# Optimization experiments

Measured on AMD Instinct MI355X. Metric: run time of the kernel, lower is better.

## Reference

```python
import jax, jax.numpy as jnp
import numpy as np

N_MICS = 192
OVERLAP = 1024
WINDOW = 524288
SPEED_OF_SOUND = 343000.0  # mm/s
FS = 768000.0


def setup_inputs() -> dict:
    key = jax.random.key(0)
    k1, k2, k3 = jax.random.split(key, 3)
    pos = jax.random.normal(k1, (1, 3), dtype=jnp.float32) * 100.0 + jnp.array([[363.0, -344.0, 1607.0]], dtype=jnp.float32)
    mic_pos = jax.random.uniform(k2, (N_MICS, 3), dtype=jnp.float32) * 100.0  # mm, spread ~100mm -> delays << OVERLAP
    buffer = jax.random.normal(k3, (N_MICS, OVERLAP + WINDOW), dtype=jnp.float32)
    return {"pos": pos, "mic_pos": mic_pos, "buffer": buffer}


def reference(pos, mic_pos, buffer):
    # distances: cdist((1,3),(M,3)) -> (M,)
    diff = pos[:, None, :] - mic_pos[None, :, :]
    distances = jnp.sqrt(jnp.sum(diff * diff, axis=-1))[0]  # (M,)
    distances = distances - distances.max()  # <= 0
    delay = -distances / SPEED_OF_SOUND * FS / 16.0  # >= 0, in samples
    delay_int = delay.astype(jnp.int32)  # trunc == floor for nonneg (matches torch .long())
    delay_frac = delay - delay_int.astype(delay.dtype)  # (M,)
    # gather indices: (M, W)
    idx = jnp.arange(WINDOW, dtype=jnp.int32)[None, :] + OVERLAP - delay_int[:, None]
    v1 = jnp.take_along_axis(buffer, idx, axis=1)       # (M, W)
    v2 = jnp.take_along_axis(buffer, idx - 1, axis=1)   # (M, W)
    f = delay_frac[:, None]
    delayed = v1 * (1.0 - f) + v2 * f
    return delayed.mean(axis=0)  # (W,)
```

## Files before the change

kernel.cpp:

```cpp
#include <hip/hip_runtime.h>

#define N_MICS  192
#define OVERLAP 1024
#define WINDOW  524288
#define ROWLEN  (OVERLAP + WINDOW)
#define BLK     256
#define SPT     4

#define RFL_I(x) __builtin_amdgcn_readfirstlane(x)
#define RFL_F(x) __uint_as_float(__builtin_amdgcn_readfirstlane(__float_as_uint(x)))

typedef float f4a4 __attribute__((ext_vector_type(4), aligned(4)));

__device__ __forceinline__ void compute_delays(
    const float* __restrict__ pos, const float* __restrict__ mic_pos,
    float* s_dist, int* s_off, float* s_df, int tid)
{
    if (tid < N_MICS) {
        float dx = __fsub_rn(pos[0], mic_pos[tid * 3 + 0]);
        float dy = __fsub_rn(pos[1], mic_pos[tid * 3 + 1]);
        float dz = __fsub_rn(pos[2], mic_pos[tid * 3 + 2]);
        float ss = __fadd_rn(__fadd_rn(__fmul_rn(dx, dx), __fmul_rn(dy, dy)),
                             __fmul_rn(dz, dz));
        s_dist[tid] = __fsqrt_rn(ss);
    }
    __syncthreads();
    if (tid < N_MICS) {
        float mx = s_dist[0];
        for (int i = 1; i < N_MICS; ++i) mx = fmaxf(mx, s_dist[i]);
        float dd = __fsub_rn(s_dist[tid], mx);
        float delay = __fmul_rn(
                          __fmul_rn(__fdiv_rn(-dd, 343000.0f), 768000.0f),
                          0.0625f);
        int di = (int)delay;
        s_off[tid] = tid * ROWLEN + OVERLAP - di;
        s_df[tid]  = __fsub_rn(delay, (float)di);
    }
    __syncthreads();
}

__global__ __launch_bounds__(BLK) void tdbf_kernel(
    const float* __restrict__ pos,
    const float* __restrict__ mic_pos,
    const float* __restrict__ buf,
    float* __restrict__ out)
{
    __shared__ float s_dist[N_MICS];
    __shared__ int   s_off[N_MICS];
    __shared__ float s_df[N_MICS];
    const int tid = threadIdx.x;
    compute_delays(pos, mic_pos, s_dist, s_off, s_df, tid);

    const int t4 = (blockIdx.x * BLK + tid) * SPT;
    float a0 = 0.f, a1 = 0.f, a2 = 0.f, a3 = 0.f;

    #pragma unroll 6
    for (int m = 0; m < N_MICS; ++m) {
        const int   off = RFL_I(s_off[m]);
        const float f   = RFL_F(s_df[m]);
        const float* p  = buf + off + t4;
        const float vm1 = p[-1];
        const f4a4  w   = *reinterpret_cast<const f4a4*>(p);
        const float g   = 1.0f - f;
        a0 = fmaf(w.x, g, fmaf(vm1, f, a0));
        a1 = fmaf(w.y, g, fmaf(w.x, f, a1));
        a2 = fmaf(w.z, g, fmaf(w.y, f, a2));
        a3 = fmaf(w.w, g, fmaf(w.z, f, a3));
    }

    const float inv = 1.0f / (float)N_MICS;
    float4 o; o.x = a0 * inv; o.y = a1 * inv; o.z = a2 * inv; o.w = a3 * inv;
    *reinterpret_cast<float4*>(out + t4) = o;
}

extern "C" void kernel_launch(void* const* d_in, const int* in_sizes, int n_in,
                              void* d_out, int out_size, void* d_ws, size_t ws_size,
                              hipStream_t stream) {
    const float* pos     = (const float*)d_in[0];
    const float* mic_pos = (const float*)d_in[1];
    const float* buf     = (const float*)d_in[2];
    float* out           = (float*)d_out;

    dim3 grid(WINDOW / (BLK * SPT));
    dim3 block(BLK);
    tdbf_kernel<<<grid, block, 0, stream>>>(pos, mic_pos, buf, out);
}
```

Measured before the change: 77.38 us.

## Split mic loop across four block groups with workspace partials and reduce kernel

```diff
diff --git a/kernel.cpp b/kernel.cpp
--- a/kernel.cpp
+++ b/kernel.cpp
@@ -6,6 +6,8 @@
 #define ROWLEN  (OVERLAP + WINDOW)
 #define BLK     256
 #define SPT     4
+#define NGRP    4
+#define MPG     (N_MICS / NGRP)
 
 #define RFL_I(x) __builtin_amdgcn_readfirstlane(x)
 #define RFL_F(x) __uint_as_float(__builtin_amdgcn_readfirstlane(__float_as_uint(x)))
@@ -39,7 +41,60 @@
     __syncthreads();
 }
 
-__global__ __launch_bounds__(BLK) void tdbf_kernel(
+__global__ __launch_bounds__(BLK) void tdbf_partial(
+    const float* __restrict__ pos,
+    const float* __restrict__ mic_pos,
+    const float* __restrict__ buf,
+    float* __restrict__ ws)
+{
+    __shared__ float s_dist[N_MICS];
+    __shared__ int   s_off[N_MICS];
+    __shared__ float s_df[N_MICS];
+    const int tid = threadIdx.x;
+    compute_delays(pos, mic_pos, s_dist, s_off, s_df, tid);
+
+    const int g    = blockIdx.y;
+    const int mBeg = g * MPG;
+    const int t4   = (blockIdx.x * BLK + tid) * SPT;
+
+    float a0 = 0.f, a1 = 0.f, a2 = 0.f, a3 = 0.f;
+
+    #pragma unroll 6
+    for (int mi = 0; mi < MPG; ++mi) {
+        const int   off = RFL_I(s_off[mBeg + mi]);
+        const float f   = RFL_F(s_df[mBeg + mi]);
+        const float* p  = buf + off + t4;
+        const float vm1 = p[-1];
+        const f4a4  w   = *reinterpret_cast<const f4a4*>(p);
+        const float gg  = 1.0f - f;
+        a0 = fmaf(w.x, gg, fmaf(vm1, f, a0));
+        a1 = fmaf(w.y, gg, fmaf(w.x, f, a1));
+        a2 = fmaf(w.z, gg, fmaf(w.y, f, a2));
+        a3 = fmaf(w.w, gg, fmaf(w.z, f, a3));
+    }
+
+    float4 o; o.x = a0; o.y = a1; o.z = a2; o.w = a3;
+    *reinterpret_cast<float4*>(ws + (size_t)g * WINDOW + t4) = o;
+}
+
+__global__ __launch_bounds__(BLK) void tdbf_reduce(
+    const float* __restrict__ ws, float* __restrict__ out)
+{
+    const int i = (blockIdx.x * BLK + threadIdx.x) * 4;
+    const float4 x0 = *reinterpret_cast<const float4*>(ws + i);
+    const float4 x1 = *reinterpret_cast<const float4*>(ws + (size_t)1 * WINDOW + i);
+    const float4 x2 = *reinterpret_cast<const float4*>(ws + (size_t)2 * WINDOW + i);
+    const float4 x3 = *reinterpret_cast<const float4*>(ws + (size_t)3 * WINDOW + i);
+    const float inv = 1.0f / (float)N_MICS;
+    float4 o;
+    o.x = (((x0.x + x1.x) + x2.x) + x3.x) * inv;
+    o.y = (((x0.y + x1.y) + x2.y) + x3.y) * inv;
+    o.z = (((x0.z + x1.z) + x2.z) + x3.z) * inv;
+    o.w = (((x0.w + x1.w) + x2.w) + x3.w) * inv;
+    *reinterpret_cast<float4*>(out + i) = o;
+}
+
+__global__ __launch_bounds__(BLK) void tdbf_mono(
     const float* __restrict__ pos,
     const float* __restrict__ mic_pos,
     const float* __restrict__ buf,
@@ -53,7 +108,6 @@
 
     const int t4 = (blockIdx.x * BLK + tid) * SPT;
     float a0 = 0.f, a1 = 0.f, a2 = 0.f, a3 = 0.f;
-
     #pragma unroll 6
     for (int m = 0; m < N_MICS; ++m) {
         const int   off = RFL_I(s_off[m]);
@@ -61,13 +115,12 @@
         const float* p  = buf + off + t4;
         const float vm1 = p[-1];
         const f4a4  w   = *reinterpret_cast<const f4a4*>(p);
-        const float g   = 1.0f - f;
-        a0 = fmaf(w.x, g, fmaf(vm1, f, a0));
-        a1 = fmaf(w.y, g, fmaf(w.x, f, a1));
-        a2 = fmaf(w.z, g, fmaf(w.y, f, a2));
-        a3 = fmaf(w.w, g, fmaf(w.z, f, a3));
+        const float gg  = 1.0f - f;
+        a0 = fmaf(w.x, gg, fmaf(vm1, f, a0));
+        a1 = fmaf(w.y, gg, fmaf(w.x, f, a1));
+        a2 = fmaf(w.z, gg, fmaf(w.y, f, a2));
+        a3 = fmaf(w.w, gg, fmaf(w.z, f, a3));
     }
-
     const float inv = 1.0f / (float)N_MICS;
     float4 o; o.x = a0 * inv; o.y = a1 * inv; o.z = a2 * inv; o.w = a3 * inv;
     *reinterpret_cast<float4*>(out + t4) = o;
@@ -81,7 +134,15 @@
     const float* buf     = (const float*)d_in[2];
     float* out           = (float*)d_out;
 
-    dim3 grid(WINDOW / (BLK * SPT));
-    dim3 block(BLK);
-    tdbf_kernel<<<grid, block, 0, stream>>>(pos, mic_pos, buf, out);
+    const size_t ws_needed = (size_t)NGRP * WINDOW * sizeof(float);
+    if (ws_size >= ws_needed) {
+        float* ws = (float*)d_ws;
+        dim3 pgrid(WINDOW / (BLK * SPT), NGRP);
+        tdbf_partial<<<pgrid, dim3(BLK), 0, stream>>>(pos, mic_pos, buf, ws);
+        dim3 rgrid(WINDOW / (BLK * 4));
+        tdbf_reduce<<<rgrid, dim3(BLK), 0, stream>>>(ws, out);
+    } else {
+        dim3 grid(WINDOW / (BLK * SPT));
+        tdbf_mono<<<grid, dim3(BLK), 0, stream>>>(pos, mic_pos, buf, out);
+    }
 }
```

Measured after the change: 85.08 us. +10.0%, slower.
